# Optimization experiments

Hardware: AMD Instinct MI355X
Metric: run time of the kernel (lower is better)

## Reference

```python
import jax, jax.numpy as jnp
import numpy as np
import math
from jax import lax

B, NP1, M, D, H, L, DFF = 16, 65, 256, 512, 8, 3, 2048
EPS_PROJ = 0.01  # MartingaleProjectionLayer is built with epsilon=0.01
LN_EPS = 1e-5


def _pos_encoding(n, d):
    pos = np.arange(n, dtype=np.float32)[:, None]
    div = np.exp(np.arange(0, d, 2, dtype=np.float32) * (-math.log(10000.0) / d))
    pe = np.zeros((n, d), dtype=np.float32)
    pe[:, 0::2] = np.sin(pos * div)
    pe[:, 1::2] = np.cos(pos * div)
    return jnp.asarray(pe)


def setup_inputs() -> dict:
    key = jax.random.key(0)
    ks = jax.random.split(key, 32)
    s = 0.02
    marg = jax.random.uniform(ks[0], (B, NP1, M), jnp.float32)
    marg = marg / marg.sum(axis=-1, keepdims=True)  # proper distributions
    return {
        "marginals": marg,
        "x_grid": jnp.linspace(-3.0, 3.0, M, dtype=jnp.float32),
        "conv_w": jax.random.normal(ks[1], (128, 1, 5), jnp.float32) * s,
        "conv_b": jax.random.normal(ks[2], (128,), jnp.float32) * s,
        "fc_w": jax.random.normal(ks[3], (128, D), jnp.float32) * s,
        "fc_b": jax.random.normal(ks[4], (D,), jnp.float32) * s,
        "ln0_g": jnp.ones((D,), jnp.float32),
        "ln0_b": jnp.zeros((D,), jnp.float32),
        "pos_enc": _pos_encoding(NP1, D),
        "qkv_w": jax.random.normal(ks[5], (L, 3 * D, D), jnp.float32) * s,
        "qkv_b": jax.random.normal(ks[6], (L, 3 * D), jnp.float32) * s,
        "out_w": jax.random.normal(ks[7], (L, D, D), jnp.float32) * s,
        "out_b": jax.random.normal(ks[8], (L, D), jnp.float32) * s,
        "ln1_g": jnp.ones((L, D), jnp.float32),
        "ln1_b": jnp.zeros((L, D), jnp.float32),
        "ff1_w": jax.random.normal(ks[9], (L, DFF, D), jnp.float32) * s,
        "ff1_b": jax.random.normal(ks[10], (L, DFF), jnp.float32) * s,
        "ff2_w": jax.random.normal(ks[11], (L, D, DFF), jnp.float32) * s,
        "ff2_b": jax.random.normal(ks[12], (L, D), jnp.float32) * s,
        "ln2_g": jnp.ones((L, D), jnp.float32),
        "ln2_b": jnp.zeros((L, D), jnp.float32),
        "u_w": jax.random.normal(ks[13], (M, D), jnp.float32) * s,
        "u_b": jax.random.normal(ks[14], (M,), jnp.float32) * s,
        "h_w": jax.random.normal(ks[15], (M, D), jnp.float32) * s,
        "h_b": jax.random.normal(ks[16], (M,), jnp.float32) * s,
    }


def _ln(x, g, b):
    mu = x.mean(axis=-1, keepdims=True)
    var = ((x - mu) ** 2).mean(axis=-1, keepdims=True)
    return (x - mu) * lax.rsqrt(var + LN_EPS) * g + b


def _gelu(x):
    return jax.nn.gelu(x, approximate=False)  # torch default exact GELU


def reference(marginals, x_grid, conv_w, conv_b, fc_w, fc_b, ln0_g, ln0_b,
              pos_enc, qkv_w, qkv_b, out_w, out_b, ln1_g, ln1_b,
              ff1_w, ff1_b, ff2_w, ff2_b, ln2_g, ln2_b, u_w, u_b, h_w, h_b):
    b, np1, m = marginals.shape
    n = np1 - 1
    d = fc_w.shape[1]
    nh = H
    dh = d // nh

    # ---- marginal embedding: Conv1d(1,128,k=5,pad=2) -> mean over grid -> FC+LN+GELU
    x = marginals.reshape(b * np1, 1, m)
    y = lax.conv_general_dilated(x, conv_w, (1,), [(2, 2)],
                                 dimension_numbers=("NCH", "OIH", "NCH"))
    y = y + conv_b[None, :, None]          # (b*np1, 128, m)
    emb = y.mean(axis=2)                   # (b*np1, 128)
    emb = _gelu(_ln(emb @ fc_w + fc_b, ln0_g, ln0_b))
    xs = emb.reshape(b, np1, d) + pos_enc[None, :np1, :]

    # ---- post-norm transformer encoder (dropout off / eval mode)
    scale = 1.0 / math.sqrt(dh)
    for l in range(L):
        qkv = xs @ qkv_w[l].T + qkv_b[l]                        # (b, s, 3d)
        q, k, v = jnp.split(qkv, 3, axis=-1)
        q = q.reshape(b, np1, nh, dh).transpose(0, 2, 1, 3)
        k = k.reshape(b, np1, nh, dh).transpose(0, 2, 1, 3)
        v = v.reshape(b, np1, nh, dh).transpose(0, 2, 1, 3)
        att = jax.nn.softmax(jnp.einsum("bhqd,bhkd->bhqk", q, k) * scale, axis=-1)
        o = jnp.einsum("bhqk,bhkd->bhqd", att, v)
        o = o.transpose(0, 2, 1, 3).reshape(b, np1, d)
        o = o @ out_w[l].T + out_b[l]
        xs = _ln(xs + o, ln1_g[l], ln1_b[l])
        ff = _gelu(xs @ ff1_w[l].T + ff1_b[l]) @ ff2_w[l].T + ff2_b[l]
        xs = _ln(xs + ff, ln2_g[l], ln2_b[l])

    u_pot = xs @ u_w.T + u_b                                    # (b, np1, M)
    h_raw = xs[:, :n, :] @ h_w.T + h_b                          # (b, n, M)

    # ---- vectorized martingale projection over all N timesteps
    x_diff = x_grid[:, None] - x_grid[None, :]                  # (M, M)
    h_kernel = h_raw[..., None] * x_diff                        # (b, n, M, M)
    P = jax.nn.softmax(h_kernel / EPS_PROJ, axis=-1)
    expected_next = jnp.einsum("bnij,j->bni", P, x_grid)
    drift = expected_next - x_grid                              # (b, n, M)
    mu = marginals[:, :n, :]
    weight_drift = (mu * drift).sum(axis=-1, keepdims=True)
    correction = weight_drift / (mu.sum(axis=-1, keepdims=True) + 1e-8)
    h_pot = h_raw - correction
    return (u_pot, h_pot)
```

## Files before the change

kernel.cpp:

```cpp
#include <hip/hip_runtime.h>
#include <math.h>


#define BT   1040
#define NP1  65
#define Dm   512
#define MG   256

typedef short short8 __attribute__((ext_vector_type(8)));
typedef float f32x4  __attribute__((ext_vector_type(4)));
typedef unsigned short u16;

__device__ __forceinline__ u16 f2bf(float f) {
  unsigned int u = __float_as_uint(f);
  u += 0x7FFF + ((u >> 16) & 1);
  return (u16)(u >> 16);
}

__device__ __forceinline__ float gelu_exact(float x) {
  return 0.5f * x * (1.0f + erff(x * 0.70710678118654752f));
}

__device__ __forceinline__ void async16(const u16* g, u16* l) {
  __builtin_amdgcn_global_load_lds(
      (const __attribute__((address_space(1))) unsigned int*)g,
      (__attribute__((address_space(3))) unsigned int*)l, 16, 0, 0);
}

__device__ __forceinline__ float wred(float v) {
#pragma unroll
  for (int o = 32; o; o >>= 1) v += __shfl_xor(v, o, 64);
  return v;
}

__device__ __forceinline__ float block_reduce_sum(float v, float* s) {
#pragma unroll
  for (int off = 32; off; off >>= 1) v += __shfl_down(v, off, 64);
  int lane = threadIdx.x & 63, wid = threadIdx.x >> 6;
  __syncthreads();
  if (lane == 0) s[wid] = v;
  __syncthreads();
  return s[0] + s[1] + s[2] + s[3];
}

__device__ __forceinline__ float f_closed(float a) {
  const float tf = 2.3529411765f;
  float t = a * tf;
  float s = fabsf(t);
  float E;
  if (s < 1e-4f) {
    E = 127.5f - 5461.25f * t;
  } else {
    float u = s * 256.0f;
    float term2 = (u < 80.0f) ? 256.0f / expm1f(u) : 0.0f;
    float Epos = 1.0f / expm1f(s) - term2;
    E = (t > 0.0f) ? Epos : 255.0f - Epos;
  }
  return -3.0f + 0.0235294118f * E;
}

__global__ __launch_bounds__(256) void prep_kernel(
    const float* __restrict__ qkv_w, const float* __restrict__ out_w,
    const float* __restrict__ ff1_w, const float* __restrict__ ff2_w,
    const float* __restrict__ u_w,   const float* __restrict__ h_w,
    u16* __restrict__ wdst,
    const float* __restrict__ marg, const float* __restrict__ conv_w,
    const float* __restrict__ conv_b, const float* __restrict__ fc_w,
    const float* __restrict__ fc_b, const float* __restrict__ g,
    const float* __restrict__ bb, const float* __restrict__ pos,
    float* __restrict__ xs, u16* __restrict__ xsb)
{
  const int tid = threadIdx.x;
  if (blockIdx.x < 512) {
    const size_t O1 = 2359296, O2 = 3145728, O3 = 6291456;
    const size_t O4 = 9437184, O5 = 9568256, TOT4 = 9699328 / 4;
    for (size_t e4 = (size_t)blockIdx.x * 256 + tid; e4 < TOT4;
         e4 += (size_t)512 * 256) {
      size_t e = e4 * 4;
      const float* src;
      if      (e < O1) src = qkv_w + e;
      else if (e < O2) src = out_w + (e - O1);
      else if (e < O3) src = ff1_w + (e - O2);
      else if (e < O4) src = ff2_w + (e - O3);
      else if (e < O5) src = u_w   + (e - O4);
      else             src = h_w   + (e - O5);
      float4 v = *(const float4*)src;
      unsigned int lo = (unsigned int)f2bf(v.x) | ((unsigned int)f2bf(v.y) << 16);
      unsigned int hi = (unsigned int)f2bf(v.z) | ((unsigned int)f2bf(v.w) << 16);
      *(uint2*)(wdst + e) = make_uint2(lo, hi);
    }
    return;
  }
  __shared__ float es[4][128];
  __shared__ float sS[4];
  __shared__ float edge[4][4];
  __shared__ float red[4];
  const int t0 = (blockIdx.x - 512) * 4;
  const int lane = tid & 63, wave = tid >> 6;
  {
    float4 mv = *(const float4*)(marg + (size_t)(t0 + wave) * MG + lane * 4);
    float S = wred(mv.x + mv.y + mv.z + mv.w);
    if (lane == 0) sS[wave] = S;
  }
  if (tid < 16) {
    int k = tid >> 2, e = tid & 3;
    int idx = (e < 2) ? e : (e + 252);
    edge[k][e] = marg[(size_t)(t0 + k) * MG + idx];
  }
  __syncthreads();
  if (tid < 128) {
    int o = tid;
    float w0 = conv_w[o*5+0], w1 = conv_w[o*5+1], w2 = conv_w[o*5+2];
    float w3 = conv_w[o*5+3], w4 = conv_w[o*5+4], cb = conv_b[o];
#pragma unroll
    for (int k = 0; k < 4; ++k) {
      float S = sS[k];
      float x0 = edge[k][0], x1 = edge[k][1], x254 = edge[k][2], x255 = edge[k][3];
      es[k][o] = (w0*(S - x254 - x255) + w1*(S - x255) + w2*S
                + w3*(S - x0) + w4*(S - x0 - x1)) * (1.0f/256.0f) + cb;
    }
  }
  __syncthreads();
  float b0 = fc_b[tid], b1 = fc_b[tid + 256];
  float z[4][2];
#pragma unroll
  for (int k = 0; k < 4; ++k) { z[k][0] = b0; z[k][1] = b1; }
#pragma unroll 4
  for (int o = 0; o < 128; ++o) {
    float f0 = fc_w[(size_t)o*Dm + tid];
    float f1 = fc_w[(size_t)o*Dm + tid + 256];
#pragma unroll
    for (int k = 0; k < 4; ++k) {
      float e = es[k][o];
      z[k][0] += e * f0; z[k][1] += e * f1;
    }
  }
  float g0 = g[tid], g1 = g[tid+256], e0 = bb[tid], e1 = bb[tid+256];
#pragma unroll
  for (int k = 0; k < 4; ++k) {
    float mu = block_reduce_sum(z[k][0] + z[k][1], red) * (1.0f/512.0f);
    float d0 = z[k][0] - mu, d1 = z[k][1] - mu;
    float var = block_reduce_sum(d0*d0 + d1*d1, red) * (1.0f/512.0f);
    float inv = rsqrtf(var + 1e-5f);
    int t = t0 + k, p = t % NP1;
    float y0 = gelu_exact(d0*inv*g0 + e0) + pos[(size_t)p*Dm + tid];
    float y1 = gelu_exact(d1*inv*g1 + e1) + pos[(size_t)p*Dm + tid + 256];
    xs[(size_t)t*Dm + tid]        = y0;
    xs[(size_t)t*Dm + tid + 256]  = y1;
    xsb[(size_t)t*Dm + tid]       = f2bf(y0);
    xsb[(size_t)t*Dm + tid + 256] = f2bf(y1);
  }
}

template<int SPLITS, int MODE>
__global__ __launch_bounds__(256) void gemm_mfma(
    const u16* __restrict__ A, const u16* __restrict__ Bw,
    const float* __restrict__ bias, float* __restrict__ Cf,
    u16* __restrict__ Cb, float* __restrict__ C2,
    const float* __restrict__ bias2, int Mrows, int N, int K)
{
  __shared__ u16 Asl[8*64*8];
  __shared__ u16 Bsl[8*64*8];
  const int tid = threadIdx.x;
  const int row0 = blockIdx.y * 64, col0 = blockIdx.x * 64;
  const int Ks = K / SPLITS, kbase = (int)blockIdx.z * Ks;
  const int lane = tid & 63, wave = tid >> 6;
  const int wm = (wave >> 1) * 32, wn = (wave & 1) * 32;
  const int l15 = lane & 15, q = lane >> 4;

  f32x4 acc[2][2];
  acc[0][0] = (f32x4){0,0,0,0}; acc[0][1] = (f32x4){0,0,0,0};
  acc[1][0] = (f32x4){0,0,0,0}; acc[1][1] = (f32x4){0,0,0,0};

  const int arow = min(row0 + lane, Mrows - 1);
  for (int k0 = kbase; k0 < kbase + Ks; k0 += 64) {
    __syncthreads();
#pragma unroll
    for (int i = 0; i < 2; ++i) {
      int c = wave * 2 + i;
      async16(A + (size_t)arow * K + k0 + c * 8,
              &Asl[(size_t)(c * 64) * 8 + lane * 8]);
      async16(Bw + (size_t)(col0 + lane) * K + k0 + c * 8,
              &Bsl[(size_t)(c * 64) * 8 + lane * 8]);
    }
    __syncthreads();
#pragma unroll
    for (int t = 0; t < 2; ++t) {
      int cc = t * 4 + q;
      short8 af[2], bf[2];
#pragma unroll
      for (int mi = 0; mi < 2; ++mi)
        af[mi] = *(short8*)&Asl[(size_t)(cc*64 + wm + mi*16 + l15) * 8];
#pragma unroll
      for (int ni = 0; ni < 2; ++ni)
        bf[ni] = *(short8*)&Bsl[(size_t)(cc*64 + wn + ni*16 + l15) * 8];
#pragma unroll
      for (int mi = 0; mi < 2; ++mi)
#pragma unroll
        for (int ni = 0; ni < 2; ++ni)
          acc[mi][ni] = __builtin_amdgcn_mfma_f32_16x16x32_bf16(
              af[mi], bf[ni], acc[mi][ni], 0, 0, 0);
    }
  }

  float* Cp = Cf;
  if (MODE == 2) Cp += (size_t)blockIdx.z * (size_t)Mrows * N;
#pragma unroll
  for (int mi = 0; mi < 2; ++mi) {
#pragma unroll
    for (int ni = 0; ni < 2; ++ni) {
      int col = col0 + wn + ni*16 + l15;
#pragma unroll
      for (int r = 0; r < 4; ++r) {
        int row = row0 + wm + mi*16 + q*4 + r;
        if (row < Mrows) {
          float v = acc[mi][ni][r];
          if (MODE == 0) {
            Cp[(size_t)row*N + col] = v + bias[col];
          } else if (MODE == 1) {
            Cb[(size_t)row*N + col] = f2bf(gelu_exact(v + bias[col]));
          } else if (MODE == 2) {
            Cp[(size_t)row*N + col] = v;
          } else {
            if (col < 256) Cf[(size_t)row*256 + col]         = v + bias[col];
            else           C2[(size_t)row*256 + (col - 256)] = v + bias2[col - 256];
          }
        }
      }
    }
  }
}

template<int S>
__global__ __launch_bounds__(256) void add_ln4(
    float* __restrict__ xs, u16* __restrict__ xsb,
    const float* __restrict__ part, const float* __restrict__ bias,
    const float* __restrict__ g, const float* __restrict__ bb)
{
  const int lane = threadIdx.x & 63, wave = threadIdx.x >> 6;
  const int t = blockIdx.x * 4 + wave;
  const int c0 = lane * 8;
  float* xp = xs + (size_t)t * Dm;
  float v[8];
  {
    float4 a0 = *(const float4*)(xp + c0), a1 = *(const float4*)(xp + c0 + 4);
    float4 b0 = *(const float4*)(bias + c0), b1 = *(const float4*)(bias + c0 + 4);
    v[0]=a0.x+b0.x; v[1]=a0.y+b0.y; v[2]=a0.z+b0.z; v[3]=a0.w+b0.w;
    v[4]=a1.x+b1.x; v[5]=a1.y+b1.y; v[6]=a1.z+b1.z; v[7]=a1.w+b1.w;
  }
#pragma unroll
  for (int s = 0; s < S; ++s) {
    const float* pp = part + (size_t)s*BT*Dm + (size_t)t*Dm + c0;
    float4 q0 = *(const float4*)pp, q1 = *(const float4*)(pp + 4);
    v[0]+=q0.x; v[1]+=q0.y; v[2]+=q0.z; v[3]+=q0.w;
    v[4]+=q1.x; v[5]+=q1.y; v[6]+=q1.z; v[7]+=q1.w;
  }
  float s1 = 0.f;
#pragma unroll
  for (int j = 0; j < 8; ++j) s1 += v[j];
  float mu = wred(s1) * (1.0f/512.0f);
  float s2 = 0.f;
#pragma unroll
  for (int j = 0; j < 8; ++j) { float d = v[j]-mu; s2 += d*d; }
  float inv = rsqrtf(wred(s2) * (1.0f/512.0f) + 1e-5f);
  float4 g0 = *(const float4*)(g + c0), g1 = *(const float4*)(g + c0 + 4);
  float4 e0 = *(const float4*)(bb + c0), e1 = *(const float4*)(bb + c0 + 4);
  float gg[8] = {g0.x,g0.y,g0.z,g0.w,g1.x,g1.y,g1.z,g1.w};
  float ee[8] = {e0.x,e0.y,e0.z,e0.w,e1.x,e1.y,e1.z,e1.w};
  float y[8]; u16 yb[8];
#pragma unroll
  for (int j = 0; j < 8; ++j) { y[j] = (v[j]-mu)*inv*gg[j] + ee[j]; yb[j] = f2bf(y[j]); }
  *(float4*)(xp + c0)     = make_float4(y[0],y[1],y[2],y[3]);
  *(float4*)(xp + c0 + 4) = make_float4(y[4],y[5],y[6],y[7]);
  *(short8*)(xsb + (size_t)t*Dm + c0) = *(short8*)yb;
}

__global__ __launch_bounds__(256) void attn_kernel(
    const float* __restrict__ qkv, u16* __restrict__ obufb)
{
  __shared__ float qv[65][67];
  __shared__ float ks[65][67];
  __shared__ float ss[65][67];
  const int b = blockIdx.x >> 3, h = blockIdx.x & 7;
  const int tid = threadIdx.x;
  const float* base = qkv + (size_t)b * NP1 * 1536 + h * 64;
  for (int idx = tid; idx < NP1 * 16; idx += 256) {
    int t = idx >> 4, c = (idx & 15) << 2;
    const float* p = base + (size_t)t * 1536 + c;
    float4 q4 = *(const float4*)(p);
    float4 k4 = *(const float4*)(p + 512);
    qv[t][c] = q4.x; qv[t][c+1] = q4.y; qv[t][c+2] = q4.z; qv[t][c+3] = q4.w;
    ks[t][c] = k4.x; ks[t][c+1] = k4.y; ks[t][c+2] = k4.z; ks[t][c+3] = k4.w;
  }
  __syncthreads();
#pragma unroll
  for (int it = 0; it < 2; ++it) {
    int tile = it * 256 + tid;
    if (tile < 289) {
      int ti = (tile / 17) * 4, tj = (tile % 17) * 4;
      const float* qr[4]; const float* kr[4];
#pragma unroll
      for (int i = 0; i < 4; ++i) { qr[i] = qv[min(ti + i, 64)]; kr[i] = ks[min(tj + i, 64)]; }
      float acc[4][4] = {};
      for (int d = 0; d < 64; ++d) {
        float a[4], bvv[4];
#pragma unroll
        for (int i = 0; i < 4; ++i) { a[i] = qr[i][d]; bvv[i] = kr[i][d]; }
#pragma unroll
        for (int i = 0; i < 4; ++i)
#pragma unroll
          for (int j = 0; j < 4; ++j) acc[i][j] += a[i] * bvv[j];
      }
#pragma unroll
      for (int i = 0; i < 4; ++i)
        if (ti + i < 65)
#pragma unroll
          for (int j = 0; j < 4; ++j)
            if (tj + j < 65) ss[ti + i][tj + j] = acc[i][j] * 0.125f;
    }
  }
  __syncthreads();
  for (int idx = tid; idx < NP1 * 16; idx += 256) {
    int t = idx >> 4, c = (idx & 15) << 2;
    float4 v4 = *(const float4*)(base + (size_t)t * 1536 + 1024 + c);
    qv[t][c] = v4.x; qv[t][c+1] = v4.y; qv[t][c+2] = v4.z; qv[t][c+3] = v4.w;
  }
  if (tid < 65) {
    float mx = -1e30f;
    for (int j = 0; j < 65; ++j) mx = fmaxf(mx, ss[tid][j]);
    float s = 0.0f;
    for (int j = 0; j < 65; ++j) { float e = expf(ss[tid][j] - mx); ss[tid][j] = e; s += e; }
    float inv = 1.0f / s;
    for (int j = 0; j < 65; ++j) ss[tid][j] *= inv;
  }
  __syncthreads();
#pragma unroll
  for (int it = 0; it < 2; ++it) {
    int tile = it * 256 + tid;
    if (tile < 272) {
      int ti = (tile >> 4) * 4, d0 = (tile & 15) * 4;
      const float* sr[4];
#pragma unroll
      for (int i = 0; i < 4; ++i) sr[i] = ss[min(ti + i, 64)];
      float acc[4][4] = {};
      for (int j = 0; j < 65; ++j) {
        float v0 = qv[j][d0], v1 = qv[j][d0+1], v2 = qv[j][d0+2], v3 = qv[j][d0+3];
#pragma unroll
        for (int i = 0; i < 4; ++i) {
          float s = sr[i][j];
          acc[i][0] += s * v0; acc[i][1] += s * v1;
          acc[i][2] += s * v2; acc[i][3] += s * v3;
        }
      }
#pragma unroll
      for (int i = 0; i < 4; ++i)
        if (ti + i < 65) {
          ushort4 o;
          o.x = f2bf(acc[i][0]); o.y = f2bf(acc[i][1]);
          o.z = f2bf(acc[i][2]); o.w = f2bf(acc[i][3]);
          *(ushort4*)(obufb + (size_t)(b * NP1 + ti + i) * Dm + h * 64 + d0) = o;
        }
    }
  }
}

__global__ __launch_bounds__(256) void proj_closed(
    const float* __restrict__ hbuf, const float* __restrict__ marg,
    const float* __restrict__ xg, float* __restrict__ out_h)
{
  const int tid = threadIdx.x, lane = tid & 63, wave = tid >> 6;
  const int rr = blockIdx.x * 4 + wave;
  const int b = rr >> 6, n = rr & 63;
  const int row = b * NP1 + n;
  const int i0 = lane * 4;
  float4 a4 = *(const float4*)(hbuf + (size_t)row * MG + i0);
  float4 x4 = *(const float4*)(xg + i0);
  float4 m4 = *(const float4*)(marg + (size_t)row * MG + i0);
  float av[4] = {a4.x, a4.y, a4.z, a4.w};
  float xv[4] = {x4.x, x4.y, x4.z, x4.w};
  float uv[4] = {m4.x, m4.y, m4.z, m4.w};
  float wd = 0.f, ms = 0.f;
#pragma unroll
  for (int k = 0; k < 4; ++k) {
    float drift = f_closed(av[k]) - xv[k];
    wd += uv[k] * drift; ms += uv[k];
  }
  wd = wred(wd); ms = wred(ms);
  float corr = wd / (ms + 1e-8f);
  *(float4*)(out_h + ((size_t)(b * 64 + n)) * MG + i0) =
      make_float4(av[0]-corr, av[1]-corr, av[2]-corr, av[3]-corr);
}

extern "C" void kernel_launch(void* const* d_in, const int* in_sizes, int n_in,
                              void* d_out, int out_size, void* d_ws, size_t ws_size,
                              hipStream_t stream)
{
  const float* marg   = (const float*)d_in[0];
  const float* xg     = (const float*)d_in[1];
  const float* conv_w = (const float*)d_in[2];
  const float* conv_b = (const float*)d_in[3];
  const float* fc_w   = (const float*)d_in[4];
  const float* fc_b   = (const float*)d_in[5];
  const float* ln0_g  = (const float*)d_in[6];
  const float* ln0_b  = (const float*)d_in[7];
  const float* pos    = (const float*)d_in[8];
  const float* qkv_w  = (const float*)d_in[9];
  const float* qkv_b  = (const float*)d_in[10];
  const float* out_w  = (const float*)d_in[11];
  const float* out_b  = (const float*)d_in[12];
  const float* ln1_g  = (const float*)d_in[13];
  const float* ln1_b  = (const float*)d_in[14];
  const float* ff1_w  = (const float*)d_in[15];
  const float* ff1_b  = (const float*)d_in[16];
  const float* ff2_w  = (const float*)d_in[17];
  const float* ff2_b  = (const float*)d_in[18];
  const float* ln2_g  = (const float*)d_in[19];
  const float* ln2_b  = (const float*)d_in[20];
  const float* u_w    = (const float*)d_in[21];
  const float* u_b    = (const float*)d_in[22];
  const float* h_w    = (const float*)d_in[23];
  const float* h_b    = (const float*)d_in[24];
  float* out = (float*)d_out;

  float* ws = (float*)d_ws;
  float* xs      = ws;
  float* qkvbuf  = ws + 532480;
  float* part    = ws + 2129920;
  float* hbuf    = ws + 4259840;
  u16*   xsb     = (u16*)(ws + 4526080);
  u16*   obufb   = (u16*)(ws + 4792320);
  u16*   ffb     = (u16*)(ws + 5058560);
  u16*   wbf     = (u16*)(ws + 6123520);

  const u16* qkv_bw = wbf;
  const u16* out_bw = wbf + 2359296;
  const u16* ff1_bw = wbf + 3145728;
  const u16* ff2_bw = wbf + 6291456;
  const u16* uh_bw  = wbf + 9437184;

  prep_kernel<<<772, 256, 0, stream>>>(
      qkv_w, out_w, ff1_w, ff2_w, u_w, h_w, wbf,
      marg, conv_w, conv_b, fc_w, fc_b, ln0_g, ln0_b, pos, xs, xsb);

  for (int l = 0; l < 3; ++l) {
    gemm_mfma<1,0><<<dim3(24, 17), 256, 0, stream>>>(
        xsb, qkv_bw + (size_t)l*786432, qkv_b + l*1536, qkvbuf,
        nullptr, nullptr, nullptr, BT, 1536, 512);
    attn_kernel<<<128, 256, 0, stream>>>(qkvbuf, obufb);
    gemm_mfma<2,2><<<dim3(8, 17, 2), 256, 0, stream>>>(
        obufb, out_bw + (size_t)l*262144, nullptr, part,
        nullptr, nullptr, nullptr, BT, 512, 512);
    add_ln4<2><<<260, 256, 0, stream>>>(xs, xsb, part, out_b + l*512,
                                        ln1_g + l*512, ln1_b + l*512);
    gemm_mfma<1,1><<<dim3(32, 17), 256, 0, stream>>>(
        xsb, ff1_bw + (size_t)l*1048576, ff1_b + l*2048, nullptr,
        ffb, nullptr, nullptr, BT, 2048, 512);
    gemm_mfma<4,2><<<dim3(8, 17, 4), 256, 0, stream>>>(
        ffb, ff2_bw + (size_t)l*1048576, nullptr, part,
        nullptr, nullptr, nullptr, BT, 512, 2048);
    add_ln4<4><<<260, 256, 0, stream>>>(xs, xsb, part, ff2_b + l*512,
                                        ln2_g + l*512, ln2_b + l*512);
  }

  gemm_mfma<1,3><<<dim3(8, 17), 256, 0, stream>>>(
      xsb, uh_bw, u_b, out, nullptr, hbuf, h_b, BT, 512, 512);
  proj_closed<<<256, 256, 0, stream>>>(hbuf, marg, xg, out + 1040*256);
}
```

Baseline: 396.9 us.

## Fuse QKV projection into attention and convert fp32 weights to bf16 inside GEMMs

Drops the separate bulk fp32-to-bf16 weight conversion pass. Each GEMM now loads fp32 weights directly and rounds them to bf16 while staging them into LDS. The QKV GEMM and the attention kernel are merged into one per-(batch, head) kernel that computes Q/K/V with MFMA into shared memory, so the fp32 qkv buffer round trip and one launch go away. In exchange, the weights are reconverted by every row-block that reads them, B loads become synchronous register loads instead of async LDS loads, and the fused attention uses only 128 blocks.

After: 504.7 us. 1.27x slower.

```diff
diff --git a/kernel.cpp b/kernel.cpp
--- a/kernel.cpp
+++ b/kernel.cpp
@@ -15,6 +15,9 @@
   unsigned int u = __float_as_uint(f);
   u += 0x7FFF + ((u >> 16) & 1);
   return (u16)(u >> 16);
+}
+__device__ __forceinline__ float bf2f(u16 v) {
+  return __uint_as_float(((unsigned int)v) << 16);
 }
 
 __device__ __forceinline__ float gelu_exact(float x) {
@@ -59,43 +62,18 @@
   return -3.0f + 0.0235294118f * E;
 }
 
-__global__ __launch_bounds__(256) void prep_kernel(
-    const float* __restrict__ qkv_w, const float* __restrict__ out_w,
-    const float* __restrict__ ff1_w, const float* __restrict__ ff2_w,
-    const float* __restrict__ u_w,   const float* __restrict__ h_w,
-    u16* __restrict__ wdst,
+__global__ __launch_bounds__(256) void embed4_kernel(
     const float* __restrict__ marg, const float* __restrict__ conv_w,
     const float* __restrict__ conv_b, const float* __restrict__ fc_w,
     const float* __restrict__ fc_b, const float* __restrict__ g,
     const float* __restrict__ bb, const float* __restrict__ pos,
     float* __restrict__ xs, u16* __restrict__ xsb)
 {
-  const int tid = threadIdx.x;
-  if (blockIdx.x < 512) {
-    const size_t O1 = 2359296, O2 = 3145728, O3 = 6291456;
-    const size_t O4 = 9437184, O5 = 9568256, TOT4 = 9699328 / 4;
-    for (size_t e4 = (size_t)blockIdx.x * 256 + tid; e4 < TOT4;
-         e4 += (size_t)512 * 256) {
-      size_t e = e4 * 4;
-      const float* src;
-      if      (e < O1) src = qkv_w + e;
-      else if (e < O2) src = out_w + (e - O1);
-      else if (e < O3) src = ff1_w + (e - O2);
-      else if (e < O4) src = ff2_w + (e - O3);
-      else if (e < O5) src = u_w   + (e - O4);
-      else             src = h_w   + (e - O5);
-      float4 v = *(const float4*)src;
-      unsigned int lo = (unsigned int)f2bf(v.x) | ((unsigned int)f2bf(v.y) << 16);
-      unsigned int hi = (unsigned int)f2bf(v.z) | ((unsigned int)f2bf(v.w) << 16);
-      *(uint2*)(wdst + e) = make_uint2(lo, hi);
-    }
-    return;
-  }
   __shared__ float es[4][128];
   __shared__ float sS[4];
   __shared__ float edge[4][4];
   __shared__ float red[4];
-  const int t0 = (blockIdx.x - 512) * 4;
+  const int t0 = blockIdx.x * 4, tid = threadIdx.x;
   const int lane = tid & 63, wave = tid >> 6;
   {
     float4 mv = *(const float4*)(marg + (size_t)(t0 + wave) * MG + lane * 4);
@@ -152,11 +130,159 @@
   }
 }
 
+struct ST { u16 Asl[8*128*8]; u16 Bsl[8*192*8]; };
+struct AT { float qs[65][67]; float ks[65][67]; u16 vs[65][68]; };
+union SMU { ST st; AT at; };
+
+__global__ __launch_bounds__(256) void attn_fused(
+    const u16* __restrict__ xsb, const float* __restrict__ Wqkv,
+    const float* __restrict__ bqkv, u16* __restrict__ obufb)
+{
+  __shared__ SMU sm;
+  __shared__ float ss[65][67];
+  const int tid = threadIdx.x, lane = tid & 63, wave = tid >> 6;
+  const int l15 = lane & 15, q4 = lane >> 4;
+  const int b = blockIdx.x >> 3, h = blockIdx.x & 7;
+  const u16* Abase = xsb + (size_t)b * NP1 * Dm;
+
+  f32x4 acc[5][3];
+#pragma unroll
+  for (int i = 0; i < 5; ++i)
+#pragma unroll
+    for (int j = 0; j < 3; ++j) acc[i][j] = (f32x4){0.f,0.f,0.f,0.f};
+
+  for (int k0 = 0; k0 < 512; k0 += 64) {
+    __syncthreads();
+#pragma unroll
+    for (int i = 0; i < 4; ++i) {
+      int idx = wave * 4 + i;
+      int c = idx >> 1, s = idx & 1;
+      int tok = min(s * 64 + lane, 64);
+      async16(Abase + (size_t)tok * Dm + k0 + c * 8,
+              &sm.st.Asl[(size_t)(c * 128 + s * 64) * 8 + lane * 8]);
+    }
+#pragma unroll
+    for (int i = 0; i < 6; ++i) {
+      int idx = wave * 6 + i;
+      int c = idx / 3, g = idx % 3;
+      const float* bp = Wqkv + (size_t)(g * 512 + h * 64 + lane) * Dm + k0 + c * 8;
+      float4 f0 = *(const float4*)bp;
+      float4 f1 = *(const float4*)(bp + 4);
+      u16 p[8] = { f2bf(f0.x), f2bf(f0.y), f2bf(f0.z), f2bf(f0.w),
+                   f2bf(f1.x), f2bf(f1.y), f2bf(f1.z), f2bf(f1.w) };
+      *(short8*)&sm.st.Bsl[(size_t)(c * 192 + g * 64 + lane) * 8] = *(short8*)p;
+    }
+    __syncthreads();
+#pragma unroll
+    for (int t = 0; t < 2; ++t) {
+      int cc = t * 4 + q4;
+      short8 af[5], bf[3];
+#pragma unroll
+      for (int mi = 0; mi < 5; ++mi)
+        af[mi] = *(short8*)&sm.st.Asl[(size_t)(cc*128 + mi*16 + l15) * 8];
+#pragma unroll
+      for (int ni = 0; ni < 3; ++ni)
+        bf[ni] = *(short8*)&sm.st.Bsl[(size_t)(cc*192 + wave*48 + ni*16 + l15) * 8];
+#pragma unroll
+      for (int mi = 0; mi < 5; ++mi)
+#pragma unroll
+        for (int ni = 0; ni < 3; ++ni)
+          acc[mi][ni] = __builtin_amdgcn_mfma_f32_16x16x32_bf16(
+              af[mi], bf[ni], acc[mi][ni], 0, 0, 0);
+    }
+  }
+  __syncthreads();
+
+#pragma unroll
+  for (int mi = 0; mi < 5; ++mi) {
+#pragma unroll
+    for (int ni = 0; ni < 3; ++ni) {
+      int col = wave * 48 + ni * 16 + l15;
+#pragma unroll
+      for (int r = 0; r < 4; ++r) {
+        int row = mi * 16 + q4 * 4 + r;
+        if (row < NP1) {
+          float v = acc[mi][ni][r];
+          if (col < 64)       sm.at.qs[row][col]       = v + bqkv[h*64 + col];
+          else if (col < 128) sm.at.ks[row][col - 64]  = v + bqkv[512 + h*64 + col - 64];
+          else                sm.at.vs[row][col - 128] = f2bf(v + bqkv[1024 + h*64 + col - 128]);
+        }
+      }
+    }
+  }
+  __syncthreads();
+
+#pragma unroll
+  for (int it = 0; it < 2; ++it) {
+    int tile = it * 256 + tid;
+    if (tile < 289) {
+      int ti = (tile / 17) * 4, tj = (tile % 17) * 4;
+      const float* qr[4]; const float* kr[4];
+#pragma unroll
+      for (int i = 0; i < 4; ++i) { qr[i] = sm.at.qs[min(ti+i,64)]; kr[i] = sm.at.ks[min(tj+i,64)]; }
+      float a2[4][4] = {};
+      for (int d = 0; d < 64; ++d) {
+        float a[4], bv[4];
+#pragma unroll
+        for (int i = 0; i < 4; ++i) { a[i] = qr[i][d]; bv[i] = kr[i][d]; }
+#pragma unroll
+        for (int i = 0; i < 4; ++i)
+#pragma unroll
+          for (int j = 0; j < 4; ++j) a2[i][j] += a[i] * bv[j];
+      }
+#pragma unroll
+      for (int i = 0; i < 4; ++i)
+        if (ti + i < NP1)
+#pragma unroll
+          for (int j = 0; j < 4; ++j)
+            if (tj + j < NP1) ss[ti+i][tj+j] = a2[i][j] * 0.125f;
+    }
+  }
+  __syncthreads();
+  if (tid < NP1) {
+    float mx = -1e30f;
+    for (int j = 0; j < NP1; ++j) mx = fmaxf(mx, ss[tid][j]);
+    float s = 0.0f;
+    for (int j = 0; j < NP1; ++j) { float e = expf(ss[tid][j] - mx); ss[tid][j] = e; s += e; }
+    float inv = 1.0f / s;
+    for (int j = 0; j < NP1; ++j) ss[tid][j] *= inv;
+  }
+  __syncthreads();
+#pragma unroll
+  for (int it = 0; it < 2; ++it) {
+    int tile = it * 256 + tid;
+    if (tile < 272) {
+      int ti = (tile >> 4) * 4, d0 = (tile & 15) * 4;
+      const float* sr[4];
+#pragma unroll
+      for (int i = 0; i < 4; ++i) sr[i] = ss[min(ti+i,64)];
+      float a2[4][4] = {};
+      for (int j = 0; j < NP1; ++j) {
+        ushort4 vv = *(const ushort4*)&sm.at.vs[j][d0];
+        float v0 = bf2f(vv.x), v1 = bf2f(vv.y), v2 = bf2f(vv.z), v3 = bf2f(vv.w);
+#pragma unroll
+        for (int i = 0; i < 4; ++i) {
+          float s = sr[i][j];
+          a2[i][0] += s*v0; a2[i][1] += s*v1; a2[i][2] += s*v2; a2[i][3] += s*v3;
+        }
+      }
+#pragma unroll
+      for (int i = 0; i < 4; ++i)
+        if (ti + i < NP1) {
+          ushort4 o;
+          o.x = f2bf(a2[i][0]); o.y = f2bf(a2[i][1]);
+          o.z = f2bf(a2[i][2]); o.w = f2bf(a2[i][3]);
+          *(ushort4*)(obufb + (size_t)(b * NP1 + ti + i) * Dm + h * 64 + d0) = o;
+        }
+    }
+  }
+}
+
 template<int SPLITS, int MODE>
-__global__ __launch_bounds__(256) void gemm_mfma(
-    const u16* __restrict__ A, const u16* __restrict__ Bw,
-    const float* __restrict__ bias, float* __restrict__ Cf,
-    u16* __restrict__ Cb, float* __restrict__ C2,
+__global__ __launch_bounds__(256) void gemm_f32b(
+    const u16* __restrict__ A, const float* __restrict__ Bw,
+    const float* __restrict__ Bw2, const float* __restrict__ bias,
+    float* __restrict__ Cf, u16* __restrict__ Cb, float* __restrict__ C2,
     const float* __restrict__ bias2, int Mrows, int N, int K)
 {
   __shared__ u16 Asl[8*64*8];
@@ -173,6 +299,10 @@
   acc[1][0] = (f32x4){0,0,0,0}; acc[1][1] = (f32x4){0,0,0,0};
 
   const int arow = min(row0 + lane, Mrows - 1);
+  const int gb = col0 + lane;
+  const float* bsrc = (MODE == 3 && gb >= 256)
+                        ? Bw2 + (size_t)(gb - 256) * K
+                        : Bw  + (size_t)gb * K;
   for (int k0 = kbase; k0 < kbase + Ks; k0 += 64) {
     __syncthreads();
 #pragma unroll
@@ -180,8 +310,12 @@
       int c = wave * 2 + i;
       async16(A + (size_t)arow * K + k0 + c * 8,
               &Asl[(size_t)(c * 64) * 8 + lane * 8]);
-      async16(Bw + (size_t)(col0 + lane) * K + k0 + c * 8,
-              &Bsl[(size_t)(c * 64) * 8 + lane * 8]);
+      const float* bp = bsrc + k0 + c * 8;
+      float4 f0 = *(const float4*)bp;
+      float4 f1 = *(const float4*)(bp + 4);
+      u16 p[8] = { f2bf(f0.x), f2bf(f0.y), f2bf(f0.z), f2bf(f0.w),
+                   f2bf(f1.x), f2bf(f1.y), f2bf(f1.z), f2bf(f1.w) };
+      *(short8*)&Bsl[(size_t)(c * 64 + lane) * 8] = *(short8*)p;
     }
     __syncthreads();
 #pragma unroll
@@ -215,9 +349,7 @@
         int row = row0 + wm + mi*16 + q*4 + r;
         if (row < Mrows) {
           float v = acc[mi][ni][r];
-          if (MODE == 0) {
-            Cp[(size_t)row*N + col] = v + bias[col];
-          } else if (MODE == 1) {
+          if (MODE == 1) {
             Cb[(size_t)row*N + col] = f2bf(gelu_exact(v + bias[col]));
           } else if (MODE == 2) {
             Cp[(size_t)row*N + col] = v;
@@ -273,95 +405,6 @@
   *(float4*)(xp + c0)     = make_float4(y[0],y[1],y[2],y[3]);
   *(float4*)(xp + c0 + 4) = make_float4(y[4],y[5],y[6],y[7]);
   *(short8*)(xsb + (size_t)t*Dm + c0) = *(short8*)yb;
-}
-
-__global__ __launch_bounds__(256) void attn_kernel(
-    const float* __restrict__ qkv, u16* __restrict__ obufb)
-{
-  __shared__ float qv[65][67];
-  __shared__ float ks[65][67];
-  __shared__ float ss[65][67];
-  const int b = blockIdx.x >> 3, h = blockIdx.x & 7;
-  const int tid = threadIdx.x;
-  const float* base = qkv + (size_t)b * NP1 * 1536 + h * 64;
-  for (int idx = tid; idx < NP1 * 16; idx += 256) {
-    int t = idx >> 4, c = (idx & 15) << 2;
-    const float* p = base + (size_t)t * 1536 + c;
-    float4 q4 = *(const float4*)(p);
-    float4 k4 = *(const float4*)(p + 512);
-    qv[t][c] = q4.x; qv[t][c+1] = q4.y; qv[t][c+2] = q4.z; qv[t][c+3] = q4.w;
-    ks[t][c] = k4.x; ks[t][c+1] = k4.y; ks[t][c+2] = k4.z; ks[t][c+3] = k4.w;
-  }
-  __syncthreads();
-#pragma unroll
-  for (int it = 0; it < 2; ++it) {
-    int tile = it * 256 + tid;
-    if (tile < 289) {
-      int ti = (tile / 17) * 4, tj = (tile % 17) * 4;
-      const float* qr[4]; const float* kr[4];
-#pragma unroll
-      for (int i = 0; i < 4; ++i) { qr[i] = qv[min(ti + i, 64)]; kr[i] = ks[min(tj + i, 64)]; }
-      float acc[4][4] = {};
-      for (int d = 0; d < 64; ++d) {
-        float a[4], bvv[4];
-#pragma unroll
-        for (int i = 0; i < 4; ++i) { a[i] = qr[i][d]; bvv[i] = kr[i][d]; }
-#pragma unroll
-        for (int i = 0; i < 4; ++i)
-#pragma unroll
-          for (int j = 0; j < 4; ++j) acc[i][j] += a[i] * bvv[j];
-      }
-#pragma unroll
-      for (int i = 0; i < 4; ++i)
-        if (ti + i < 65)
-#pragma unroll
-          for (int j = 0; j < 4; ++j)
-            if (tj + j < 65) ss[ti + i][tj + j] = acc[i][j] * 0.125f;
-    }
-  }
-  __syncthreads();
-  for (int idx = tid; idx < NP1 * 16; idx += 256) {
-    int t = idx >> 4, c = (idx & 15) << 2;
-    float4 v4 = *(const float4*)(base + (size_t)t * 1536 + 1024 + c);
-    qv[t][c] = v4.x; qv[t][c+1] = v4.y; qv[t][c+2] = v4.z; qv[t][c+3] = v4.w;
-  }
-  if (tid < 65) {
-    float mx = -1e30f;
-    for (int j = 0; j < 65; ++j) mx = fmaxf(mx, ss[tid][j]);
-    float s = 0.0f;
-    for (int j = 0; j < 65; ++j) { float e = expf(ss[tid][j] - mx); ss[tid][j] = e; s += e; }
-    float inv = 1.0f / s;
-    for (int j = 0; j < 65; ++j) ss[tid][j] *= inv;
-  }
-  __syncthreads();
-#pragma unroll
-  for (int it = 0; it < 2; ++it) {
-    int tile = it * 256 + tid;
-    if (tile < 272) {
-      int ti = (tile >> 4) * 4, d0 = (tile & 15) * 4;
-      const float* sr[4];
-#pragma unroll
-      for (int i = 0; i < 4; ++i) sr[i] = ss[min(ti + i, 64)];
-      float acc[4][4] = {};
-      for (int j = 0; j < 65; ++j) {
-        float v0 = qv[j][d0], v1 = qv[j][d0+1], v2 = qv[j][d0+2], v3 = qv[j][d0+3];
-#pragma unroll
-        for (int i = 0; i < 4; ++i) {
-          float s = sr[i][j];
-          acc[i][0] += s * v0; acc[i][1] += s * v1;
-          acc[i][2] += s * v2; acc[i][3] += s * v3;
-        }
-      }
-#pragma unroll
-      for (int i = 0; i < 4; ++i)
-        if (ti + i < 65) {
-          ushort4 o;
-          o.x = f2bf(acc[i][0]); o.y = f2bf(acc[i][1]);
-          o.z = f2bf(acc[i][2]); o.w = f2bf(acc[i][3]);
-          *(ushort4*)(obufb + (size_t)(b * NP1 + ti + i) * Dm + h * 64 + d0) = o;
-        }
-    }
-  }
 }
 
 __global__ __launch_bounds__(256) void proj_closed(
@@ -424,45 +467,34 @@
 
   float* ws = (float*)d_ws;
   float* xs      = ws;
-  float* qkvbuf  = ws + 532480;
-  float* part    = ws + 2129920;
-  float* hbuf    = ws + 4259840;
-  u16*   xsb     = (u16*)(ws + 4526080);
-  u16*   obufb   = (u16*)(ws + 4792320);
-  u16*   ffb     = (u16*)(ws + 5058560);
-  u16*   wbf     = (u16*)(ws + 6123520);
-
-  const u16* qkv_bw = wbf;
-  const u16* out_bw = wbf + 2359296;
-  const u16* ff1_bw = wbf + 3145728;
-  const u16* ff2_bw = wbf + 6291456;
-  const u16* uh_bw  = wbf + 9437184;
-
-  prep_kernel<<<772, 256, 0, stream>>>(
-      qkv_w, out_w, ff1_w, ff2_w, u_w, h_w, wbf,
-      marg, conv_w, conv_b, fc_w, fc_b, ln0_g, ln0_b, pos, xs, xsb);
+  float* part    = ws + 532480;
+  float* hbuf    = ws + 2662400;
+  u16*   xsb     = (u16*)(ws + 2928640);
+  u16*   obufb   = (u16*)(ws + 3194880);
+  u16*   ffb     = (u16*)(ws + 3461120);
+
+  embed4_kernel<<<260, 256, 0, stream>>>(marg, conv_w, conv_b, fc_w, fc_b,
+                                         ln0_g, ln0_b, pos, xs, xsb);
 
   for (int l = 0; l < 3; ++l) {
-    gemm_mfma<1,0><<<dim3(24, 17), 256, 0, stream>>>(
-        xsb, qkv_bw + (size_t)l*786432, qkv_b + l*1536, qkvbuf,
-        nullptr, nullptr, nullptr, BT, 1536, 512);
-    attn_kernel<<<128, 256, 0, stream>>>(qkvbuf, obufb);
-    gemm_mfma<2,2><<<dim3(8, 17, 2), 256, 0, stream>>>(
-        obufb, out_bw + (size_t)l*262144, nullptr, part,
+    attn_fused<<<128, 256, 0, stream>>>(
+        xsb, qkv_w + (size_t)l*786432, qkv_b + l*1536, obufb);
+    gemm_f32b<2,2><<<dim3(8, 17, 2), 256, 0, stream>>>(
+        obufb, out_w + (size_t)l*262144, nullptr, nullptr, part,
         nullptr, nullptr, nullptr, BT, 512, 512);
     add_ln4<2><<<260, 256, 0, stream>>>(xs, xsb, part, out_b + l*512,
                                         ln1_g + l*512, ln1_b + l*512);
-    gemm_mfma<1,1><<<dim3(32, 17), 256, 0, stream>>>(
-        xsb, ff1_bw + (size_t)l*1048576, ff1_b + l*2048, nullptr,
+    gemm_f32b<1,1><<<dim3(32, 17), 256, 0, stream>>>(
+        xsb, ff1_w + (size_t)l*1048576, nullptr, ff1_b + l*2048, nullptr,
         ffb, nullptr, nullptr, BT, 2048, 512);
-    gemm_mfma<4,2><<<dim3(8, 17, 4), 256, 0, stream>>>(
-        ffb, ff2_bw + (size_t)l*1048576, nullptr, part,
+    gemm_f32b<4,2><<<dim3(8, 17, 4), 256, 0, stream>>>(
+        ffb, ff2_w + (size_t)l*1048576, nullptr, nullptr, part,
         nullptr, nullptr, nullptr, BT, 512, 2048);
     add_ln4<4><<<260, 256, 0, stream>>>(xs, xsb, part, ff2_b + l*512,
                                         ln2_g + l*512, ln2_b + l*512);
   }
 
-  gemm_mfma<1,3><<<dim3(8, 17), 256, 0, stream>>>(
-      xsb, uh_bw, u_b, out, nullptr, hbuf, h_b, BT, 512, 512);
+  gemm_f32b<1,3><<<dim3(8, 17), 256, 0, stream>>>(
+      xsb, u_w, h_w, u_b, out, nullptr, hbuf, h_b, BT, 512, 512);
   proj_closed<<<256, 256, 0, stream>>>(hbuf, marg, xg, out + 1040*256);
 }
```

## Convert fp32 weights to bf16 inside GEMM loads and store QKV as bf16

Applied to the files above, without the earlier changes.

Removes the upfront prep pass that converted every weight matrix to bf16 in workspace. Each GEMM now reads fp32 weights directly and converts them to bf16 in registers before staging to shared memory, replacing the async global-to-LDS copy for B. The QKV output is stored as bf16 and the attention kernel reads bf16. This avoids one full read and write of the weights, but doubles the weight bytes each GEMM reads and re-converts weights once per row-tile block, which adds ALU work and loses the async load path.

Result: slower. 459.9 us (+15.9%).

```diff
diff --git a/kernel.cpp b/kernel.cpp
--- a/kernel.cpp
+++ b/kernel.cpp
@@ -15,6 +15,9 @@
   unsigned int u = __float_as_uint(f);
   u += 0x7FFF + ((u >> 16) & 1);
   return (u16)(u >> 16);
+}
+__device__ __forceinline__ float bf2f(u16 v) {
+  return __uint_as_float(((unsigned int)v) << 16);
 }
 
 __device__ __forceinline__ float gelu_exact(float x) {
@@ -59,43 +62,18 @@
   return -3.0f + 0.0235294118f * E;
 }
 
-__global__ __launch_bounds__(256) void prep_kernel(
-    const float* __restrict__ qkv_w, const float* __restrict__ out_w,
-    const float* __restrict__ ff1_w, const float* __restrict__ ff2_w,
-    const float* __restrict__ u_w,   const float* __restrict__ h_w,
-    u16* __restrict__ wdst,
+__global__ __launch_bounds__(256) void embed4_kernel(
     const float* __restrict__ marg, const float* __restrict__ conv_w,
     const float* __restrict__ conv_b, const float* __restrict__ fc_w,
     const float* __restrict__ fc_b, const float* __restrict__ g,
     const float* __restrict__ bb, const float* __restrict__ pos,
     float* __restrict__ xs, u16* __restrict__ xsb)
 {
-  const int tid = threadIdx.x;
-  if (blockIdx.x < 512) {
-    const size_t O1 = 2359296, O2 = 3145728, O3 = 6291456;
-    const size_t O4 = 9437184, O5 = 9568256, TOT4 = 9699328 / 4;
-    for (size_t e4 = (size_t)blockIdx.x * 256 + tid; e4 < TOT4;
-         e4 += (size_t)512 * 256) {
-      size_t e = e4 * 4;
-      const float* src;
-      if      (e < O1) src = qkv_w + e;
-      else if (e < O2) src = out_w + (e - O1);
-      else if (e < O3) src = ff1_w + (e - O2);
-      else if (e < O4) src = ff2_w + (e - O3);
-      else if (e < O5) src = u_w   + (e - O4);
-      else             src = h_w   + (e - O5);
-      float4 v = *(const float4*)src;
-      unsigned int lo = (unsigned int)f2bf(v.x) | ((unsigned int)f2bf(v.y) << 16);
-      unsigned int hi = (unsigned int)f2bf(v.z) | ((unsigned int)f2bf(v.w) << 16);
-      *(uint2*)(wdst + e) = make_uint2(lo, hi);
-    }
-    return;
-  }
   __shared__ float es[4][128];
   __shared__ float sS[4];
   __shared__ float edge[4][4];
   __shared__ float red[4];
-  const int t0 = (blockIdx.x - 512) * 4;
+  const int t0 = blockIdx.x * 4, tid = threadIdx.x;
   const int lane = tid & 63, wave = tid >> 6;
   {
     float4 mv = *(const float4*)(marg + (size_t)(t0 + wave) * MG + lane * 4);
@@ -153,10 +131,10 @@
 }
 
 template<int SPLITS, int MODE>
-__global__ __launch_bounds__(256) void gemm_mfma(
-    const u16* __restrict__ A, const u16* __restrict__ Bw,
-    const float* __restrict__ bias, float* __restrict__ Cf,
-    u16* __restrict__ Cb, float* __restrict__ C2,
+__global__ __launch_bounds__(256) void gemm_f32b(
+    const u16* __restrict__ A, const float* __restrict__ Bw,
+    const float* __restrict__ Bw2, const float* __restrict__ bias,
+    float* __restrict__ Cf, u16* __restrict__ Cb, float* __restrict__ C2,
     const float* __restrict__ bias2, int Mrows, int N, int K)
 {
   __shared__ u16 Asl[8*64*8];
@@ -173,6 +151,10 @@
   acc[1][0] = (f32x4){0,0,0,0}; acc[1][1] = (f32x4){0,0,0,0};
 
   const int arow = min(row0 + lane, Mrows - 1);
+  const int gb = col0 + lane;
+  const float* bsrc = (MODE == 3 && gb >= 256)
+                        ? Bw2 + (size_t)(gb - 256) * K
+                        : Bw  + (size_t)gb * K;
   for (int k0 = kbase; k0 < kbase + Ks; k0 += 64) {
     __syncthreads();
 #pragma unroll
@@ -180,8 +162,12 @@
       int c = wave * 2 + i;
       async16(A + (size_t)arow * K + k0 + c * 8,
               &Asl[(size_t)(c * 64) * 8 + lane * 8]);
-      async16(Bw + (size_t)(col0 + lane) * K + k0 + c * 8,
-              &Bsl[(size_t)(c * 64) * 8 + lane * 8]);
+      const float* bp = bsrc + k0 + c * 8;
+      float4 f0 = *(const float4*)bp;
+      float4 f1 = *(const float4*)(bp + 4);
+      u16 p[8] = { f2bf(f0.x), f2bf(f0.y), f2bf(f0.z), f2bf(f0.w),
+                   f2bf(f1.x), f2bf(f1.y), f2bf(f1.z), f2bf(f1.w) };
+      *(short8*)&Bsl[(size_t)(c * 64 + lane) * 8] = *(short8*)p;
     }
     __syncthreads();
 #pragma unroll
@@ -216,7 +202,7 @@
         if (row < Mrows) {
           float v = acc[mi][ni][r];
           if (MODE == 0) {
-            Cp[(size_t)row*N + col] = v + bias[col];
+            Cb[(size_t)row*N + col] = f2bf(v + bias[col]);
           } else if (MODE == 1) {
             Cb[(size_t)row*N + col] = f2bf(gelu_exact(v + bias[col]));
           } else if (MODE == 2) {
@@ -231,6 +217,98 @@
   }
 }
 
+__global__ __launch_bounds__(256) void attn_kernel(
+    const u16* __restrict__ qkvb, u16* __restrict__ obufb)
+{
+  __shared__ float qv[65][67];
+  __shared__ float ks[65][67];
+  __shared__ float ss[65][67];
+  const int b = blockIdx.x >> 3, h = blockIdx.x & 7;
+  const int tid = threadIdx.x;
+  const u16* base = qkvb + (size_t)b * NP1 * 1536 + h * 64;
+  for (int idx = tid; idx < NP1 * 16; idx += 256) {
+    int t = idx >> 4, c = (idx & 15) << 2;
+    const u16* p = base + (size_t)t * 1536 + c;
+    ushort4 q4 = *(const ushort4*)(p);
+    ushort4 k4 = *(const ushort4*)(p + 512);
+    qv[t][c] = bf2f(q4.x); qv[t][c+1] = bf2f(q4.y);
+    qv[t][c+2] = bf2f(q4.z); qv[t][c+3] = bf2f(q4.w);
+    ks[t][c] = bf2f(k4.x); ks[t][c+1] = bf2f(k4.y);
+    ks[t][c+2] = bf2f(k4.z); ks[t][c+3] = bf2f(k4.w);
+  }
+  __syncthreads();
+#pragma unroll
+  for (int it = 0; it < 2; ++it) {
+    int tile = it * 256 + tid;
+    if (tile < 289) {
+      int ti = (tile / 17) * 4, tj = (tile % 17) * 4;
+      const float* qr[4]; const float* kr[4];
+#pragma unroll
+      for (int i = 0; i < 4; ++i) { qr[i] = qv[min(ti + i, 64)]; kr[i] = ks[min(tj + i, 64)]; }
+      float acc[4][4] = {};
+      for (int d = 0; d < 64; ++d) {
+        float a[4], bvv[4];
+#pragma unroll
+        for (int i = 0; i < 4; ++i) { a[i] = qr[i][d]; bvv[i] = kr[i][d]; }
+#pragma unroll
+        for (int i = 0; i < 4; ++i)
+#pragma unroll
+          for (int j = 0; j < 4; ++j) acc[i][j] += a[i] * bvv[j];
+      }
+#pragma unroll
+      for (int i = 0; i < 4; ++i)
+        if (ti + i < 65)
+#pragma unroll
+          for (int j = 0; j < 4; ++j)
+            if (tj + j < 65) ss[ti + i][tj + j] = acc[i][j] * 0.125f;
+    }
+  }
+  __syncthreads();
+  for (int idx = tid; idx < NP1 * 16; idx += 256) {
+    int t = idx >> 4, c = (idx & 15) << 2;
+    ushort4 v4 = *(const ushort4*)(base + (size_t)t * 1536 + 1024 + c);
+    qv[t][c] = bf2f(v4.x); qv[t][c+1] = bf2f(v4.y);
+    qv[t][c+2] = bf2f(v4.z); qv[t][c+3] = bf2f(v4.w);
+  }
+  if (tid < 65) {
+    float mx = -1e30f;
+    for (int j = 0; j < 65; ++j) mx = fmaxf(mx, ss[tid][j]);
+    float s = 0.0f;
+    for (int j = 0; j < 65; ++j) { float e = expf(ss[tid][j] - mx); ss[tid][j] = e; s += e; }
+    float inv = 1.0f / s;
+    for (int j = 0; j < 65; ++j) ss[tid][j] *= inv;
+  }
+  __syncthreads();
+#pragma unroll
+  for (int it = 0; it < 2; ++it) {
+    int tile = it * 256 + tid;
+    if (tile < 272) {
+      int ti = (tile >> 4) * 4, d0 = (tile & 15) * 4;
+      const float* sr[4];
+#pragma unroll
+      for (int i = 0; i < 4; ++i) sr[i] = ss[min(ti + i, 64)];
+      float acc[4][4] = {};
+      for (int j = 0; j < 65; ++j) {
+        float v0 = qv[j][d0], v1 = qv[j][d0+1], v2 = qv[j][d0+2], v3 = qv[j][d0+3];
+#pragma unroll
+        for (int i = 0; i < 4; ++i) {
+          float s = sr[i][j];
+          acc[i][0] += s * v0; acc[i][1] += s * v1;
+          acc[i][2] += s * v2; acc[i][3] += s * v3;
+        }
+      }
+#pragma unroll
+      for (int i = 0; i < 4; ++i)
+        if (ti + i < 65) {
+          ushort4 o;
+          o.x = f2bf(acc[i][0]); o.y = f2bf(acc[i][1]);
+          o.z = f2bf(acc[i][2]); o.w = f2bf(acc[i][3]);
+          *(ushort4*)(obufb + (size_t)(b * NP1 + ti + i) * Dm + h * 64 + d0) = o;
+        }
+    }
+  }
+}
+
 template<int S>
 __global__ __launch_bounds__(256) void add_ln4(
     float* __restrict__ xs, u16* __restrict__ xsb,
@@ -273,95 +351,6 @@
   *(float4*)(xp + c0)     = make_float4(y[0],y[1],y[2],y[3]);
   *(float4*)(xp + c0 + 4) = make_float4(y[4],y[5],y[6],y[7]);
   *(short8*)(xsb + (size_t)t*Dm + c0) = *(short8*)yb;
-}
-
-__global__ __launch_bounds__(256) void attn_kernel(
-    const float* __restrict__ qkv, u16* __restrict__ obufb)
-{
-  __shared__ float qv[65][67];
-  __shared__ float ks[65][67];
-  __shared__ float ss[65][67];
-  const int b = blockIdx.x >> 3, h = blockIdx.x & 7;
-  const int tid = threadIdx.x;
-  const float* base = qkv + (size_t)b * NP1 * 1536 + h * 64;
-  for (int idx = tid; idx < NP1 * 16; idx += 256) {
-    int t = idx >> 4, c = (idx & 15) << 2;
-    const float* p = base + (size_t)t * 1536 + c;
-    float4 q4 = *(const float4*)(p);
-    float4 k4 = *(const float4*)(p + 512);
-    qv[t][c] = q4.x; qv[t][c+1] = q4.y; qv[t][c+2] = q4.z; qv[t][c+3] = q4.w;
-    ks[t][c] = k4.x; ks[t][c+1] = k4.y; ks[t][c+2] = k4.z; ks[t][c+3] = k4.w;
-  }
-  __syncthreads();
-#pragma unroll
-  for (int it = 0; it < 2; ++it) {
-    int tile = it * 256 + tid;
-    if (tile < 289) {
-      int ti = (tile / 17) * 4, tj = (tile % 17) * 4;
-      const float* qr[4]; const float* kr[4];
-#pragma unroll
-      for (int i = 0; i < 4; ++i) { qr[i] = qv[min(ti + i, 64)]; kr[i] = ks[min(tj + i, 64)]; }
-      float acc[4][4] = {};
-      for (int d = 0; d < 64; ++d) {
-        float a[4], bvv[4];
-#pragma unroll
-        for (int i = 0; i < 4; ++i) { a[i] = qr[i][d]; bvv[i] = kr[i][d]; }
-#pragma unroll
-        for (int i = 0; i < 4; ++i)
-#pragma unroll
-          for (int j = 0; j < 4; ++j) acc[i][j] += a[i] * bvv[j];
-      }
-#pragma unroll
-      for (int i = 0; i < 4; ++i)
-        if (ti + i < 65)
-#pragma unroll
-          for (int j = 0; j < 4; ++j)
-            if (tj + j < 65) ss[ti + i][tj + j] = acc[i][j] * 0.125f;
-    }
-  }
-  __syncthreads();
-  for (int idx = tid; idx < NP1 * 16; idx += 256) {
-    int t = idx >> 4, c = (idx & 15) << 2;
-    float4 v4 = *(const float4*)(base + (size_t)t * 1536 + 1024 + c);
-    qv[t][c] = v4.x; qv[t][c+1] = v4.y; qv[t][c+2] = v4.z; qv[t][c+3] = v4.w;
-  }
-  if (tid < 65) {
-    float mx = -1e30f;
-    for (int j = 0; j < 65; ++j) mx = fmaxf(mx, ss[tid][j]);
-    float s = 0.0f;
-    for (int j = 0; j < 65; ++j) { float e = expf(ss[tid][j] - mx); ss[tid][j] = e; s += e; }
-    float inv = 1.0f / s;
-    for (int j = 0; j < 65; ++j) ss[tid][j] *= inv;
-  }
-  __syncthreads();
-#pragma unroll
-  for (int it = 0; it < 2; ++it) {
-    int tile = it * 256 + tid;
-    if (tile < 272) {
-      int ti = (tile >> 4) * 4, d0 = (tile & 15) * 4;
-      const float* sr[4];
-#pragma unroll
-      for (int i = 0; i < 4; ++i) sr[i] = ss[min(ti + i, 64)];
-      float acc[4][4] = {};
-      for (int j = 0; j < 65; ++j) {
-        float v0 = qv[j][d0], v1 = qv[j][d0+1], v2 = qv[j][d0+2], v3 = qv[j][d0+3];
-#pragma unroll
-        for (int i = 0; i < 4; ++i) {
-          float s = sr[i][j];
-          acc[i][0] += s * v0; acc[i][1] += s * v1;
-          acc[i][2] += s * v2; acc[i][3] += s * v3;
-        }
-      }
-#pragma unroll
-      for (int i = 0; i < 4; ++i)
-        if (ti + i < 65) {
-          ushort4 o;
-          o.x = f2bf(acc[i][0]); o.y = f2bf(acc[i][1]);
-          o.z = f2bf(acc[i][2]); o.w = f2bf(acc[i][3]);
-          *(ushort4*)(obufb + (size_t)(b * NP1 + ti + i) * Dm + h * 64 + d0) = o;
-        }
-    }
-  }
 }
 
 __global__ __launch_bounds__(256) void proj_closed(
@@ -424,45 +413,37 @@
 
   float* ws = (float*)d_ws;
   float* xs      = ws;
-  float* qkvbuf  = ws + 532480;
-  float* part    = ws + 2129920;
-  float* hbuf    = ws + 4259840;
-  u16*   xsb     = (u16*)(ws + 4526080);
-  u16*   obufb   = (u16*)(ws + 4792320);
-  u16*   ffb     = (u16*)(ws + 5058560);
-  u16*   wbf     = (u16*)(ws + 6123520);
-
-  const u16* qkv_bw = wbf;
-  const u16* out_bw = wbf + 2359296;
-  const u16* ff1_bw = wbf + 3145728;
-  const u16* ff2_bw = wbf + 6291456;
-  const u16* uh_bw  = wbf + 9437184;
-
-  prep_kernel<<<772, 256, 0, stream>>>(
-      qkv_w, out_w, ff1_w, ff2_w, u_w, h_w, wbf,
-      marg, conv_w, conv_b, fc_w, fc_b, ln0_g, ln0_b, pos, xs, xsb);
+  float* part    = ws + 532480;
+  float* hbuf    = ws + 2662400;
+  u16*   xsb     = (u16*)(ws + 2928640);
+  u16*   obufb   = (u16*)(ws + 3194880);
+  u16*   ffb     = (u16*)(ws + 3461120);
+  u16*   qkvb    = (u16*)(ws + 4526080);
+
+  embed4_kernel<<<260, 256, 0, stream>>>(marg, conv_w, conv_b, fc_w, fc_b,
+                                         ln0_g, ln0_b, pos, xs, xsb);
 
   for (int l = 0; l < 3; ++l) {
-    gemm_mfma<1,0><<<dim3(24, 17), 256, 0, stream>>>(
-        xsb, qkv_bw + (size_t)l*786432, qkv_b + l*1536, qkvbuf,
-        nullptr, nullptr, nullptr, BT, 1536, 512);
-    attn_kernel<<<128, 256, 0, stream>>>(qkvbuf, obufb);
-    gemm_mfma<2,2><<<dim3(8, 17, 2), 256, 0, stream>>>(
-        obufb, out_bw + (size_t)l*262144, nullptr, part,
+    gemm_f32b<1,0><<<dim3(24, 17), 256, 0, stream>>>(
+        xsb, qkv_w + (size_t)l*786432, nullptr, qkv_b + l*1536,
+        nullptr, qkvb, nullptr, nullptr, BT, 1536, 512);
+    attn_kernel<<<128, 256, 0, stream>>>(qkvb, obufb);
+    gemm_f32b<2,2><<<dim3(8, 17, 2), 256, 0, stream>>>(
+        obufb, out_w + (size_t)l*262144, nullptr, nullptr, part,
         nullptr, nullptr, nullptr, BT, 512, 512);
     add_ln4<2><<<260, 256, 0, stream>>>(xs, xsb, part, out_b + l*512,
                                         ln1_g + l*512, ln1_b + l*512);
-    gemm_mfma<1,1><<<dim3(32, 17), 256, 0, stream>>>(
-        xsb, ff1_bw + (size_t)l*1048576, ff1_b + l*2048, nullptr,
+    gemm_f32b<1,1><<<dim3(32, 17), 256, 0, stream>>>(
+        xsb, ff1_w + (size_t)l*1048576, nullptr, ff1_b + l*2048, nullptr,
         ffb, nullptr, nullptr, BT, 2048, 512);
-    gemm_mfma<4,2><<<dim3(8, 17, 4), 256, 0, stream>>>(
-        ffb, ff2_bw + (size_t)l*1048576, nullptr, part,
+    gemm_f32b<4,2><<<dim3(8, 17, 4), 256, 0, stream>>>(
+        ffb, ff2_w + (size_t)l*1048576, nullptr, nullptr, part,
         nullptr, nullptr, nullptr, BT, 512, 2048);
     add_ln4<4><<<260, 256, 0, stream>>>(xs, xsb, part, ff2_b + l*512,
                                         ln2_g + l*512, ln2_b + l*512);
   }
 
-  gemm_mfma<1,3><<<dim3(8, 17), 256, 0, stream>>>(
-      xsb, uh_bw, u_b, out, nullptr, hbuf, h_b, BT, 512, 512);
+  gemm_f32b<1,3><<<dim3(8, 17), 256, 0, stream>>>(
+      xsb, u_w, h_w, u_b, out, nullptr, hbuf, h_b, BT, 512, 512);
   proj_closed<<<256, 256, 0, stream>>>(hbuf, marg, xg, out + 1040*256);
 }
```
